# Performance work log

Measured on AMD Instinct MI355X. Metric: run time of the kernel, lower is better.

The kernel has to match this reference:

```python
import jax, jax.numpy as jnp
import numpy as np

V, E, H, B, S, T, NE, NC = 50000, 300, 150, 64, 16, 48, 100001, 300


def bigru(x, Wih, Whh, bih, bhh):
    # x: [T, N, D]; PyTorch GRU cell math, bidirectional -> [T, N, 2H]
    outs = []
    for d in range(2):
        def step(h, xt, d=d):
            gi = xt @ Wih[d].T + bih[d]
            gh = h @ Whh[d].T + bhh[d]
            ir, iz, inn = jnp.split(gi, 3, axis=-1)
            hr, hz, hn = jnp.split(gh, 3, axis=-1)
            r = jax.nn.sigmoid(ir + hr)
            z = jax.nn.sigmoid(iz + hz)
            n = jnp.tanh(inn + r * hn)
            h2 = (1.0 - z) * n + z * h
            return h2, h2
        h0 = jnp.zeros((x.shape[1], Whh.shape[-1]), x.dtype)
        _, hs = jax.lax.scan(step, h0, x, reverse=(d == 1))
        outs.append(hs)
    return jnp.concatenate(outs, axis=-1)


def attend(hs, W, b, ctx):
    # hs: [T, N, G]; softmax attention over time axis
    u = jnp.tanh(jnp.einsum('tng,hg->tnh', hs, W) + b)
    a = jax.nn.softmax(jnp.einsum('tnh,h->tn', u, ctx), axis=0)
    return jnp.einsum('tn,tng->ng', a, hs)


def cos_sim(a, c, eps=1e-8):
    # a: [B, D], c: [B, K, D] -> [B, K]  (torch.cosine_similarity semantics)
    num = jnp.einsum('bd,bkd->bk', a, c)
    den = jnp.linalg.norm(a, axis=-1, keepdims=True) * jnp.linalg.norm(c, axis=-1)
    return num / jnp.maximum(den, eps)


def setup_inputs() -> dict:
    key = jax.random.key(0)
    ks = jax.random.split(key, 20)
    nrm = lambda k, s: (jax.random.normal(k, s, jnp.float32) * 0.05)
    return {
        'docs': jax.random.randint(ks[0], (B, S, T), 0, V),
        'sens': jax.random.randint(ks[1], (B,), 0, S),
        'candidates': jax.random.randint(ks[2], (B, 1, NC), 0, NE),
        'idx': jax.random.randint(ks[3], (B,), 1, NC + 1),  # 1-based gold id
        'word_emb': nrm(ks[4], (V, E)),
        'ent_emb': nrm(ks[5], (NE, E)),
        'Wih_w': nrm(ks[6], (2, 3 * H, E)),
        'Whh_w': nrm(ks[7], (2, 3 * H, H)),
        'bih_w': jnp.zeros((2, 3 * H), jnp.float32),
        'bhh_w': jnp.zeros((2, 3 * H), jnp.float32),
        'attW_w': nrm(ks[8], (2 * H, 2 * H)),
        'attb_w': jnp.zeros((2 * H,), jnp.float32),
        'ctx_w': nrm(ks[9], (2 * H,)),
        'Wih_s': nrm(ks[10], (2, 3 * H, 2 * H)),
        'Whh_s': nrm(ks[11], (2, 3 * H, H)),
        'bih_s': jnp.zeros((2, 3 * H), jnp.float32),
        'bhh_s': jnp.zeros((2, 3 * H), jnp.float32),
        'attW_s': nrm(ks[12], (2 * H, 2 * H)),
        'attb_s': jnp.zeros((2 * H,), jnp.float32),
        'ctx_s': nrm(ks[13], (2 * H,)),
        'linW': nrm(ks[14], (NC, 2 * NC)),
        'linb': jnp.zeros((NC,), jnp.float32),
    }


def reference(docs, sens, candidates, idx, word_emb, ent_emb,
              Wih_w, Whh_w, bih_w, bhh_w, attW_w, attb_w, ctx_w,
              Wih_s, Whh_s, bih_s, bhh_s, attW_s, attb_s, ctx_s,
              linW, linb):
    b, s, t = docs.shape
    # ---- word-level encoder over every sentence at once ----
    x = word_emb[docs]                              # [B,S,T,E]
    x = x.transpose(2, 0, 1, 3).reshape(t, b * s, E)  # [T, B*S, E]
    hs = bigru(x, Wih_w, Whh_w, bih_w, bhh_w)       # [T, B*S, 2H]
    sent_vec = attend(hs, attW_w, attb_w, ctx_w)    # [B*S, 2H]
    sent_vec = sent_vec.reshape(b, s, 2 * H)        # output_per_sen.permute(1,0,2)
    output_sen = sent_vec[jnp.arange(b), sens]      # [B, 2H] mention sentence
    # ---- sentence-level encoder ----
    xs = sent_vec.transpose(1, 0, 2)                # [S, B, 2H]
    hss = bigru(xs, Wih_s, Whh_s, bih_s, bhh_s)     # [S, B, 2H]
    output_doc = attend(hss, attW_s, attb_s, ctx_s)  # [B, 2H]
    # ---- batched cosine similarity against candidate entity embeddings ----
    can = ent_emb[candidates[:, 0]]                 # [B, NC, E]
    sim_total = jnp.concatenate([cos_sim(output_sen, can), cos_sim(output_doc, can)], axis=1)  # [B, 2*NC]
    score = sim_total @ linW.T + linb               # [B, NC]
    score_gold = score[jnp.arange(b), idx - 1]      # [B]
    max_index = jnp.argmax(score, axis=1)           # [B]
    return (score_gold, score, max_index)
```

## Files before the change

### kernel.cpp

```cpp
#include <hip/hip_runtime.h>
#include <hip/hip_bf16.h>
#include <math.h>

#define B_  64
#define S_  16
#define T_  48
#define E_  300
#define H_  150
#define G_  300
#define NC_ 300
#define NW_ (B_*S_)
#define RW_ (T_*NW_)
#define RS_ (S_*B_)
#define GST 960

typedef __attribute__((ext_vector_type(8))) short bf16x8;
typedef __attribute__((ext_vector_type(4))) float f32x4;

__device__ __forceinline__ float sigm(float x){ return 1.0f/(1.0f+__expf(-x)); }

__device__ __forceinline__ ushort f2bf_rne(float x){
  uint u = __float_as_uint(x);
  return (ushort)((u + 0x7FFFu + ((u>>16)&1u)) >> 16);
}

__global__ __launch_bounds__(256) void prep_whh_kernel(
    const float* __restrict__ Whh, float* __restrict__ Wblk){
  int idx = blockIdx.x*256 + threadIdx.x;
  if (idx >= 2*38*450*4) return;
  int k  = idx & 3;
  int j  = (idx >> 2) % 450;
  int e4 = (idx >> 2) / 450 % 38;
  int d  = idx / (38*450*4);
  int e  = e4*4 + k;
  Wblk[idx] = (e < 150) ? Whh[((size_t)d*450 + j)*150 + e] : 0.f;
}

__global__ __launch_bounds__(256) void prep_whh_mfma(
    const float* __restrict__ Whh, ushort* __restrict__ Bsh,
    ushort* __restrict__ Bsl){
  int idx = blockIdx.x*256 + threadIdx.x;
  if (idx >= 2*512*160) return;
  int k = idx % 160;
  int j = (idx / 160) % 512;
  int d = idx / (512*160);
  float x = (j < 450 && k < 150) ? Whh[((size_t)d*450 + j)*150 + k] : 0.f;
  ushort hb = f2bf_rne(x);
  Bsh[idx] = hb;
  Bsl[idx] = f2bf_rne(x - __uint_as_float(((uint)hb)<<16));
}

__global__ __launch_bounds__(128) void split_w_gen(
    const float* __restrict__ W, ushort* __restrict__ Whi,
    ushort* __restrict__ Wlo, int R, int C, int Cp){
  int j = blockIdx.x;
  for (int k = threadIdx.x; k < Cp; k += 128){
    float x = (j < R && k < C) ? W[(size_t)j*C + k] : 0.f;
    ushort hb = f2bf_rne(x);
    float hf = __uint_as_float(((uint)hb)<<16);
    Whi[(size_t)j*Cp + k] = hb;
    Wlo[(size_t)j*Cp + k] = f2bf_rne(x - hf);
  }
}

__global__ __launch_bounds__(256) void gi_mfma_v4(
    const int* __restrict__ docs, const float* __restrict__ emb,
    const ushort* __restrict__ Whi, const ushort* __restrict__ Wlo,
    const float* __restrict__ bih, float* __restrict__ gi){
  __shared__ __align__(16) ushort Bhi[16*328];
  __shared__ __align__(16) ushort Blo[16*328];
  __shared__ __align__(16) float  Cst[64*68];
  __shared__ int toks[64];
  int tid = threadIdx.x;
  int gr0 = blockIdx.x * 64;
  int t  = gr0 >> 10;
  int n0 = gr0 & 1023;
  if (tid < 64) toks[tid] = docs[(n0 + tid)*T_ + t];
  uint4 pb[5];
#pragma unroll
  for (int i=0;i<5;i++){
    int c = tid + i*256;
    int half = (c >= 640) ? 1 : 0; int cc = c - half*640;
    int row = cc/40, o16 = cc - row*40;
    const ushort* src = half ? Wlo : Whi;
    pb[i] = *(const uint4*)&src[(size_t)row*320 + o16*8];
  }
  __syncthreads();
  int w = tid >> 6, L = tid & 63;
  int lrow = L & 15, lseg = L >> 4;
  const float* aptr = emb + (size_t)toks[w*16 + lrow]*300;
  bf16x8 ah[10], al[10];
#pragma unroll
  for (int ks=0; ks<10; ks++){
    int k0 = ks*32 + lseg*8;
    float x[8];
    if (k0 + 8 <= 300){
      float4 v0 = *(const float4*)&aptr[k0];
      float4 v1 = *(const float4*)&aptr[k0+4];
      x[0]=v0.x; x[1]=v0.y; x[2]=v0.z; x[3]=v0.w;
      x[4]=v1.x; x[5]=v1.y; x[6]=v1.z; x[7]=v1.w;
    } else {
#pragma unroll
      for (int u=0;u<8;u++) x[u] = (k0+u < 300) ? aptr[k0+u] : 0.f;
    }
#pragma unroll
    for (int u=0;u<8;u++){
      ushort hb = f2bf_rne(x[u]);
      float lo = x[u] - __uint_as_float(((uint)hb)<<16);
      ah[ks][u] = (short)hb;
      al[ks][u] = (short)f2bf_rne(lo);
    }
  }
#pragma unroll
  for (int i=0;i<5;i++){
    int c = tid + i*256;
    int half = (c >= 640) ? 1 : 0; int cc = c - half*640;
    int row = cc/40, o16 = cc - row*40;
    ushort* dst = half ? Blo : Bhi;
    *(uint4*)&dst[row*328 + o16*8] = pb[i];
  }
  __syncthreads();
  int bfb = lrow*328 + lseg*8;
  int rl0 = w*16 + lseg*4;
  f32x4 acc4[4];
  for (int g = 0; g < 14; ++g){
#pragma unroll
    for (int q = 0; q < 4; ++q){
      int nt = g*4 + q;
#pragma unroll
      for (int i=0;i<5;i++){
        int c = tid + i*256;
        int half = (c >= 640) ? 1 : 0; int cc = c - half*640;
        int row = cc/40, o16 = cc - row*40;
        const ushort* src = half ? Wlo : Whi;
        pb[i] = *(const uint4*)&src[(size_t)((nt+1)*16 + row)*320 + o16*8];
      }
      f32x4 acc = {0.f, 0.f, 0.f, 0.f};
#pragma unroll
      for (int ks=0; ks<10; ks++){
        bf16x8 bh = *(const bf16x8*)&Bhi[bfb + ks*32];
        bf16x8 bl = *(const bf16x8*)&Blo[bfb + ks*32];
        acc = __builtin_amdgcn_mfma_f32_16x16x32_bf16(ah[ks], bh, acc, 0, 0, 0);
        acc = __builtin_amdgcn_mfma_f32_16x16x32_bf16(ah[ks], bl, acc, 0, 0, 0);
        acc = __builtin_amdgcn_mfma_f32_16x16x32_bf16(al[ks], bh, acc, 0, 0, 0);
      }
      acc4[q] = acc;
      __syncthreads();
#pragma unroll
      for (int i=0;i<5;i++){
        int c = tid + i*256;
        int half = (c >= 640) ? 1 : 0; int cc = c - half*640;
        int row = cc/40, o16 = cc - row*40;
        ushort* dst = half ? Blo : Bhi;
        *(uint4*)&dst[row*328 + o16*8] = pb[i];
      }
      __syncthreads();
    }
#pragma unroll
    for (int q = 0; q < 4; ++q){
#pragma unroll
      for (int r = 0; r < 4; ++r)
        Cst[(rl0 + r)*68 + q*16 + lrow] = acc4[q][r];
    }
    __syncthreads();
#pragma unroll
    for (int i = 0; i < 4; ++i){
      int idxc = tid + i*256;
      int row = idxc >> 4, c4 = idxc & 15;
      int colb = g*64 + c4*4;
      float4 v = *(float4*)&Cst[row*68 + c4*4];
      float4 bb = *(const float4*)&bih[colb];
      v.x += bb.x; v.y += bb.y; v.z += bb.z; v.w += bb.w;
      *(float4*)&gi[(size_t)(gr0 + row)*GST + colb] = v;
    }
  }
  {
    f32x4 acc = {0.f, 0.f, 0.f, 0.f};
#pragma unroll
    for (int ks=0; ks<10; ks++){
      bf16x8 bh = *(const bf16x8*)&Bhi[bfb + ks*32];
      bf16x8 bl = *(const bf16x8*)&Blo[bfb + ks*32];
      acc = __builtin_amdgcn_mfma_f32_16x16x32_bf16(ah[ks], bh, acc, 0, 0, 0);
      acc = __builtin_amdgcn_mfma_f32_16x16x32_bf16(ah[ks], bl, acc, 0, 0, 0);
      acc = __builtin_amdgcn_mfma_f32_16x16x32_bf16(al[ks], bh, acc, 0, 0, 0);
    }
    int col = 896 + lrow;
    if (col < 900){
      float bb = bih[col];
#pragma unroll
      for (int r=0;r<4;r++)
        gi[(size_t)(gr0 + rl0 + r)*GST + col] = acc[r] + bb;
    }
  }
}

__global__ __launch_bounds__(256,3) void att_mfma_kernel(
    const float* __restrict__ hs, const ushort* __restrict__ Whi,
    const ushort* __restrict__ Wlo, const float* __restrict__ bias,
    const float* __restrict__ ctx, float* __restrict__ score, int Rtot){
  __shared__ __align__(16) ushort Bhi[2][16*328];
  __shared__ __align__(16) ushort Blo[2][16*328];
  int tid = threadIdx.x;
  int r0 = blockIdx.x * 64;
  uint4 pb[5];
#pragma unroll
  for (int i=0;i<5;i++){
    int c = tid + i*256;
    int half = (c >= 640) ? 1 : 0; int cc = c - half*640;
    int row = cc/40, o16 = cc - row*40;
    const ushort* src = half ? Wlo : Whi;
    pb[i] = *(const uint4*)&src[(size_t)row*320 + o16*8];
  }
  int w = tid >> 6, L = tid & 63;
  int lrow = L & 15, lseg = L >> 4;
  int arow = r0 + w*16 + lrow;
  bool avalid = arow < Rtot;
  const float* aptr = hs + (size_t)(avalid ? arow : 0)*300;
  bf16x8 ah[10], al[10];
#pragma unroll
  for (int ks=0; ks<10; ks++){
    int k0 = ks*32 + lseg*8;
    float x[8];
    if (avalid && k0 + 8 <= 300){
      float4 v0 = *(const float4*)&aptr[k0];
      float4 v1 = *(const float4*)&aptr[k0+4];
      x[0]=v0.x; x[1]=v0.y; x[2]=v0.z; x[3]=v0.w;
      x[4]=v1.x; x[5]=v1.y; x[6]=v1.z; x[7]=v1.w;
    } else {
#pragma unroll
      for (int u=0;u<8;u++) x[u] = (avalid && k0+u < 300) ? aptr[k0+u] : 0.f;
    }
#pragma unroll
    for (int u=0;u<8;u++){
      ushort hb = f2bf_rne(x[u]);
      float lo = x[u] - __uint_as_float(((uint)hb)<<16);
      ah[ks][u] = (short)hb;
      al[ks][u] = (short)f2bf_rne(lo);
    }
  }
#pragma unroll
  for (int i=0;i<5;i++){
    int c = tid + i*256;
    int half = (c >= 640) ? 1 : 0; int cc = c - half*640;
    int row = cc/40, o16 = cc - row*40;
    ushort* dst = half ? Blo[0] : Bhi[0];
    *(uint4*)&dst[row*328 + o16*8] = pb[i];
  }
  __syncthreads();
  int buf = 0;
  int bfb = lrow*328 + lseg*8;
  float part[4] = {0.f,0.f,0.f,0.f};
  for (int nt = 0; nt < 19; ++nt){
    if (nt < 18){
#pragma unroll
      for (int i=0;i<5;i++){
        int c = tid + i*256;
        int half = (c >= 640) ? 1 : 0; int cc = c - half*640;
        int row = cc/40, o16 = cc - row*40;
        const ushort* src = half ? Wlo : Whi;
        pb[i] = *(const uint4*)&src[(size_t)((nt+1)*16 + row)*320 + o16*8];
      }
    }
    f32x4 acc = {0.f, 0.f, 0.f, 0.f};
#pragma unroll
    for (int ks=0; ks<10; ks++){
      bf16x8 bh = *(const bf16x8*)&Bhi[buf][bfb + ks*32];
      bf16x8 bl = *(const bf16x8*)&Blo[buf][bfb + ks*32];
      acc = __builtin_amdgcn_mfma_f32_16x16x32_bf16(ah[ks], bh, acc, 0, 0, 0);
      acc = __builtin_amdgcn_mfma_f32_16x16x32_bf16(ah[ks], bl, acc, 0, 0, 0);
      acc = __builtin_amdgcn_mfma_f32_16x16x32_bf16(al[ks], bh, acc, 0, 0, 0);
    }
    int col = nt*16 + lrow;
    if (col < 300){
      float bb = bias[col], cx = ctx[col];
#pragma unroll
      for (int r=0;r<4;r++) part[r] += cx * tanhf(acc[r] + bb);
    }
    if (nt < 18){
#pragma unroll
      for (int i=0;i<5;i++){
        int c = tid + i*256;
        int half = (c >= 640) ? 1 : 0; int cc = c - half*640;
        int row = cc/40, o16 = cc - row*40;
        ushort* dst = half ? Blo[buf^1] : Bhi[buf^1];
        *(uint4*)&dst[row*328 + o16*8] = pb[i];
      }
    }
    __syncthreads();
    buf ^= 1;
  }
#pragma unroll
  for (int off=1; off<16; off<<=1){
#pragma unroll
    for (int r=0;r<4;r++) part[r] += __shfl_xor(part[r], off);
  }
  if (lrow == 0){
    int rbase = r0 + w*16 + lseg*4;
#pragma unroll
    for (int r=0;r<4;r++)
      if (rbase + r < Rtot) score[rbase + r] = part[r];
  }
}

__global__ __launch_bounds__(256) void sent_gi_kernel(
    const float* __restrict__ sv, const float* __restrict__ Wih,
    const float* __restrict__ bih, float* __restrict__ gi){
  __shared__ float A[16][G_];
  int r0 = blockIdx.x * 16;
  int s  = r0 >> 6;
  int bb_ = r0 & 63;
  for (int idx = threadIdx.x; idx < 16*75; idx += 256){
    int row = idx / 75, e4 = idx - row*75;
    *(float4*)&A[row][e4*4] =
        *(const float4*)&sv[(((size_t)(bb_+row))*S_ + s)*G_ + e4*4];
  }
  __syncthreads();
  int q = threadIdx.x;
  if (q >= 225) return;
  int j0 = q*4;
  const float4* w0 = (const float4*)(Wih + (size_t)(j0  )*G_);
  const float4* w1 = (const float4*)(Wih + (size_t)(j0+1)*G_);
  const float4* w2 = (const float4*)(Wih + (size_t)(j0+2)*G_);
  const float4* w3 = (const float4*)(Wih + (size_t)(j0+3)*G_);
  float acc[16][4];
#pragma unroll
  for (int i=0;i<16;i++){ acc[i][0]=0.f; acc[i][1]=0.f; acc[i][2]=0.f; acc[i][3]=0.f; }
  for (int e4=0; e4<75; e4++){
    float4 b0=w0[e4], b1=w1[e4], b2=w2[e4], b3=w3[e4];
#pragma unroll
    for (int i=0;i<16;i++){
      float4 av = *(const float4*)&A[i][e4*4];
      acc[i][0] += av.x*b0.x + av.y*b0.y + av.z*b0.z + av.w*b0.w;
      acc[i][1] += av.x*b1.x + av.y*b1.y + av.z*b1.z + av.w*b1.w;
      acc[i][2] += av.x*b2.x + av.y*b2.y + av.z*b2.z + av.w*b2.w;
      acc[i][3] += av.x*b3.x + av.y*b3.y + av.z*b3.z + av.w*b3.w;
    }
  }
  float4 bb = *(const float4*)&bih[j0];
#pragma unroll
  for (int i=0;i<16;i++){
    float4 o4;
    o4.x = acc[i][0]+bb.x; o4.y = acc[i][1]+bb.y;
    o4.z = acc[i][2]+bb.z; o4.w = acc[i][3]+bb.w;
    *(float4*)&gi[((size_t)(s*B_) + bb_ + i)*GST + j0] = o4;
  }
}

__global__ __launch_bounds__(512,2) void gru_mfma2(
    const float* __restrict__ gi, const ushort* __restrict__ Bsh,
    const ushort* __restrict__ Bsl, const float* __restrict__ bhh,
    float* __restrict__ hs, int T, int N){
  __shared__ __align__(16) ushort Ahi[16*168];
  __shared__ __align__(16) ushort Alo[16*168];
  __shared__ float gh[16*468];
  __shared__ float lds_pad[10240];
  int tid = threadIdx.x;
  int d  = blockIdx.y;
  int n0 = blockIdx.x * 8;
  if (N == -12345) lds_pad[tid] = 0.f;
  for (int i = tid; i < 16*168; i += 512){ Ahi[i] = 0; Alo[i] = 0; }
  int wv = tid >> 6, L = tid & 63;
  int lrow = L & 15, lseg = L >> 4;
  bf16x8 Bh[4][5], Bl[4][5];
  {
    const ushort* bh_ = Bsh + (size_t)d*512*160;
    const ushort* bl_ = Bsl + (size_t)d*512*160;
#pragma unroll
    for (int q=0;q<4;q++){
      int row = (wv + q*8)*16 + lrow;
#pragma unroll
      for (int ks=0;ks<5;ks++){
        Bh[q][ks] = *(const bf16x8*)&bh_[(size_t)row*160 + lseg*8 + ks*32];
        Bl[q][ks] = *(const bf16x8*)&bl_[(size_t)row*160 + lseg*8 + ks*32];
      }
    }
  }
  int erow[3], eh[3];
  float bb_r[3], bb_z[3], bb_n[3], hold[3];
#pragma unroll
  for (int r=0;r<3;r++){
    int e = tid + r*512;
    bool v = e < 1200;
    int e2 = v ? e : 0;
    erow[r] = e2 / 150; eh[r] = e2 % 150;
    bb_r[r] = v ? bhh[d*450 + eh[r]]        : 0.f;
    bb_z[r] = v ? bhh[d*450 + 150 + eh[r]]  : 0.f;
    bb_n[r] = v ? bhh[d*450 + 300 + eh[r]]  : 0.f;
    hold[r] = 0.f;
  }
  __syncthreads();
  for (int step = 0; step < T; ++step){
    int t = d ? (T-1-step) : step;
    bf16x8 Ah[5], Al[5];
#pragma unroll
    for (int ks=0;ks<5;ks++){
      Ah[ks] = *(const bf16x8*)&Ahi[lrow*168 + lseg*8 + ks*32];
      Al[ks] = *(const bf16x8*)&Alo[lrow*168 + lseg*8 + ks*32];
    }
#pragma unroll
    for (int q=0;q<4;q++){
      int nt = wv + q*8;
      if (nt < 29){
        f32x4 acc = {0.f,0.f,0.f,0.f};
#pragma unroll
        for (int ks=0;ks<5;ks++){
          acc = __builtin_amdgcn_mfma_f32_16x16x32_bf16(Ah[ks], Bh[q][ks], acc, 0,0,0);
          acc = __builtin_amdgcn_mfma_f32_16x16x32_bf16(Ah[ks], Bl[q][ks], acc, 0,0,0);
          acc = __builtin_amdgcn_mfma_f32_16x16x32_bf16(Al[ks], Bh[q][ks], acc, 0,0,0);
        }
        int col = nt*16 + lrow;
#pragma unroll
        for (int r=0;r<4;r++)
          gh[(lseg*4 + r)*468 + col] = acc[r];
      }
    }
    const float* gib = gi + ((size_t)t*N + n0)*GST + d*450;
    float pr[3], pz[3], pn[3];
#pragma unroll
    for (int r=0;r<3;r++){
      if (tid + r*512 < 1200){
        const float* g0 = gib + (size_t)erow[r]*GST + eh[r];
        pr[r] = g0[0]; pz[r] = g0[150]; pn[r] = g0[300];
      }
    }
    __syncthreads();
#pragma unroll
    for (int r=0;r<3;r++){
      if (tid + r*512 < 1200){
        int row = erow[r], h = eh[r];
        float ghr = gh[row*468 + h];
        float ghz = gh[row*468 + 150 + h];
        float ghn = gh[row*468 + 300 + h];
        float rr = sigm(pr[r] + ghr + bb_r[r]);
        float zz = sigm(pz[r] + ghz + bb_z[r]);
        float nn = tanhf(pn[r] + rr*(ghn + bb_n[r]));
        float h2 = (1.f - zz)*nn + zz*hold[r];
        hold[r] = h2;
        ushort hb = f2bf_rne(h2);
        Ahi[row*168 + h] = hb;
        Alo[row*168 + h] = f2bf_rne(h2 - __uint_as_float(((uint)hb)<<16));
        hs[((size_t)t*N + n0 + row)*G_ + d*H_ + h] = h2;
      }
    }
    __syncthreads();
  }
}

template<int R>
__global__ __launch_bounds__(512,2) void gru_scan_v4(
    const float* __restrict__ gi, const float* __restrict__ Wblk,
    const float* __restrict__ bhh, float* __restrict__ hs,
    int T, int N){
  int d  = blockIdx.y;
  int n0 = blockIdx.x * R;
  __shared__ float hl[2][R][152];
  __shared__ float gh[R][452];
  int tid = threadIdx.x;
  for (int idx = tid; idx < 2*R*152; idx += 512) (&hl[0][0][0])[idx] = 0.f;
  bool jact = tid < 450;
  bool hact = tid < 150;
  float4 Wr[38];
  float bj = 0.f;
  {
    const float4* Wb4 = (const float4*)(Wblk + (size_t)d*38*1800);
    int jj = jact ? tid : 0;
#pragma unroll
    for (int e4 = 0; e4 < 38; ++e4) Wr[e4] = Wb4[e4*450 + jj];
    if (jact) bj = bhh[d*450 + tid];
  }
  float hreg[R];
#pragma unroll
  for (int i=0;i<R;i++) hreg[i] = 0.f;
  int buf = 0;
  __syncthreads();
  for (int step = 0; step < T; ++step){
    int t = d ? (T-1-step) : step;
    const float* gib = gi + ((size_t)t*N + n0)*GST + d*450;
    float pre[R][3];
    if (hact){
#pragma unroll
      for (int i=0;i<R;i++){
        pre[i][0] = gib[(size_t)i*GST + tid];
        pre[i][1] = gib[(size_t)i*GST + 150 + tid];
        pre[i][2] = gib[(size_t)i*GST + 300 + tid];
      }
    }
    if (jact){
      float acc[R];
#pragma unroll
      for (int i=0;i<R;i++) acc[i] = 0.f;
#pragma unroll
      for (int e4 = 0; e4 < 38; ++e4){
        float4 w = Wr[e4];
#pragma unroll
        for (int i=0;i<R;i++){
          float4 hv = *(const float4*)&hl[buf][i][e4*4];
          acc[i] += w.x*hv.x + w.y*hv.y + w.z*hv.z + w.w*hv.w;
        }
      }
#pragma unroll
      for (int i=0;i<R;i++) gh[i][tid] = acc[i] + bj;
    }
    __syncthreads();
    if (hact){
#pragma unroll
      for (int i=0;i<R;i++){
        float r  = sigm(pre[i][0] + gh[i][tid]);
        float z  = sigm(pre[i][1] + gh[i][150+tid]);
        float nn = tanhf(pre[i][2] + r*gh[i][300+tid]);
        float h2 = (1.f - z)*nn + z*hreg[i];
        hreg[i] = h2;
        hl[buf^1][i][tid] = h2;
        hs[((size_t)t*N + n0 + i)*G_ + d*H_ + tid] = h2;
      }
    }
    buf ^= 1;
    __syncthreads();
  }
}

__global__ __launch_bounds__(256) void att_combine_kernel(
    const float* __restrict__ score, const float* __restrict__ hs,
    float* __restrict__ out, int T, int N){
  int n = blockIdx.x;
  __shared__ float wa[64];
  if (threadIdx.x < T) wa[threadIdx.x] = score[threadIdx.x*N + n];
  __syncthreads();
  float m = -1e30f;
  for (int t=0;t<T;t++) m = fmaxf(m, wa[t]);
  float den = 0.f;
  for (int t=0;t<T;t++) den += __expf(wa[t]-m);
  float inv = 1.f/den;
  __syncthreads();
  if (threadIdx.x < T) wa[threadIdx.x] = __expf(wa[threadIdx.x]-m)*inv;
  __syncthreads();
  for (int g = threadIdx.x; g < G_; g += 256){
    float acc = 0.f;
    for (int t=0;t<T;t++) acc += wa[t] * hs[((size_t)t*N+n)*G_ + g];
    out[(size_t)n*G_ + g] = acc;
  }
}

__global__ __launch_bounds__(256) void cossim_kernel(
    const int* __restrict__ cand, const int* __restrict__ sens,
    const float* __restrict__ ent, const float* __restrict__ sv,
    const float* __restrict__ odoc, float* __restrict__ sim){
  int w = (blockIdx.x*256 + threadIdx.x) >> 6;
  int lane = threadIdx.x & 63;
  if (w >= B_*NC_) return;
  int b = w / NC_, k = w - b*NC_;
  const float* c  = ent + (size_t)cand[b*NC_ + k]*E_;
  const float* a1 = sv  + ((size_t)b*S_ + sens[b])*G_;
  const float* a2 = odoc + (size_t)b*G_;
  float d1=0.f,d2=0.f,cc=0.f,n1=0.f,n2=0.f;
  for (int e = lane; e < E_; e += 64){
    float cv=c[e], v1=a1[e], v2=a2[e];
    d1+=v1*cv; d2+=v2*cv; cc+=cv*cv; n1+=v1*v1; n2+=v2*v2;
  }
  for (int off=32; off; off>>=1){
    d1+=__shfl_xor(d1,off); d2+=__shfl_xor(d2,off); cc+=__shfl_xor(cc,off);
    n1+=__shfl_xor(n1,off); n2+=__shfl_xor(n2,off);
  }
  if (lane == 0){
    float nc = sqrtf(cc);
    sim[(size_t)b*600 + k]       = d1 / fmaxf(sqrtf(n1)*nc, 1e-8f);
    sim[(size_t)b*600 + 300 + k] = d2 / fmaxf(sqrtf(n2)*nc, 1e-8f);
  }
}

__global__ __launch_bounds__(256) void final_kernel(
    const float* __restrict__ sim, const float* __restrict__ linW,
    const float* __restrict__ linb, const int* __restrict__ idx,
    float* __restrict__ out){
  int b = blockIdx.x;
  __shared__ float ss[600];
  __shared__ float sc[300];
  __shared__ float bv[256];
  __shared__ int   bi[256];
  for (int j = threadIdx.x; j < 600; j += 256) ss[j] = sim[(size_t)b*600 + j];
  __syncthreads();
  float bestv = -1e30f; int besti = 0;
  for (int i = threadIdx.x; i < 300; i += 256){
    const float4* wr = (const float4*)(linW + (size_t)i*600);
    float acc = linb[i];
    for (int j4=0; j4<150; j4++){
      float4 w = wr[j4];
      int j = j4*4;
      acc += w.x*ss[j] + w.y*ss[j+1] + w.z*ss[j+2] + w.w*ss[j+3];
    }
    sc[i] = acc;
    out[64 + (size_t)b*300 + i] = acc;
    if (acc > bestv){ bestv = acc; besti = i; }
  }
  bv[threadIdx.x] = bestv; bi[threadIdx.x] = besti;
  __syncthreads();
  for (int s=128; s; s>>=1){
    if (threadIdx.x < s){
      float ov = bv[threadIdx.x+s]; int oi = bi[threadIdx.x+s];
      if (ov > bv[threadIdx.x] || (ov == bv[threadIdx.x] && oi < bi[threadIdx.x])){
        bv[threadIdx.x] = ov; bi[threadIdx.x] = oi;
      }
    }
    __syncthreads();
  }
  if (threadIdx.x == 0){
    out[b] = sc[idx[b]-1];
    out[64 + 64*300 + b] = (float)bi[0];
  }
}

extern "C" void kernel_launch(void* const* d_in, const int* in_sizes, int n_in,
                              void* d_out, int out_size, void* d_ws, size_t ws_size,
                              hipStream_t stream){
  const int*   docs  = (const int*)d_in[0];
  const int*   sens  = (const int*)d_in[1];
  const int*   cand  = (const int*)d_in[2];
  const int*   idx   = (const int*)d_in[3];
  const float* wemb  = (const float*)d_in[4];
  const float* eemb  = (const float*)d_in[5];
  const float* Wih_w = (const float*)d_in[6];
  const float* Whh_w = (const float*)d_in[7];
  const float* bih_w = (const float*)d_in[8];
  const float* bhh_w = (const float*)d_in[9];
  const float* attW_w= (const float*)d_in[10];
  const float* attb_w= (const float*)d_in[11];
  const float* ctx_w = (const float*)d_in[12];
  const float* Wih_s = (const float*)d_in[13];
  const float* Whh_s = (const float*)d_in[14];
  const float* bih_s = (const float*)d_in[15];
  const float* bhh_s = (const float*)d_in[16];
  const float* attW_s= (const float*)d_in[17];
  const float* attb_s= (const float*)d_in[18];
  const float* ctx_s = (const float*)d_in[19];
  const float* linW  = (const float*)d_in[20];
  const float* linb  = (const float*)d_in[21];

  float* ws = (float*)d_ws;
  size_t off = 0;
  float* gi_w    = ws + off; off += (size_t)T_*NW_*GST;
  float* hs_w    = ws + off; off += (size_t)T_*NW_*G_;
  float* score_w = ws + off; off += (size_t)T_*NW_;
  float* sv      = ws + off; off += (size_t)NW_*G_;
  float* hs_s    = ws + off; off += (size_t)S_*B_*G_;
  float* score_s = ws + off; off += (size_t)S_*B_;
  float* odoc    = ws + off; off += (size_t)B_*G_;
  float* sim     = ws + off; off += (size_t)B_*600;
  float* Wblk_s  = ws + off; off += (size_t)2*38*450*4;
  ushort* Whi    = (ushort*)(ws + off); off += (size_t)912*320/2;
  ushort* Wlo    = (ushort*)(ws + off); off += (size_t)912*320/2;
  ushort* WAhi   = (ushort*)(ws + off); off += (size_t)304*320/2;
  ushort* WAlo   = (ushort*)(ws + off); off += (size_t)304*320/2;
  ushort* WShi   = (ushort*)(ws + off); off += (size_t)304*320/2;
  ushort* WSlo   = (ushort*)(ws + off); off += (size_t)304*320/2;
  ushort* Bsh    = (ushort*)(ws + off); off += (size_t)2*512*160/2;
  ushort* Bsl    = (ushort*)(ws + off); off += (size_t)2*512*160/2;
  float* gi_s    = gi_w;

  float* out = (float*)d_out;

  prep_whh_kernel<<<(2*38*450*4+255)/256, 256, 0, stream>>>(Whh_s, Wblk_s);
  prep_whh_mfma<<<(2*512*160+255)/256, 256, 0, stream>>>(Whh_w, Bsh, Bsl);
  split_w_gen<<<912, 128, 0, stream>>>(Wih_w, Whi, Wlo, 900, 300, 320);
  split_w_gen<<<304, 128, 0, stream>>>(attW_w, WAhi, WAlo, 300, 300, 320);
  split_w_gen<<<304, 128, 0, stream>>>(attW_s, WShi, WSlo, 300, 300, 320);

  gi_mfma_v4<<<RW_/64, 256, 0, stream>>>(docs, wemb, Whi, Wlo, bih_w, gi_w);
  gru_mfma2<<<dim3(NW_/8, 2), 512, 0, stream>>>(gi_w, Bsh, Bsl, bhh_w,
                                                hs_w, T_, NW_);
  att_mfma_kernel<<<RW_/64, 256, 0, stream>>>(hs_w, WAhi, WAlo, attb_w,
                                              ctx_w, score_w, RW_);
  att_combine_kernel<<<NW_, 256, 0, stream>>>(score_w, hs_w, sv, T_, NW_);

  sent_gi_kernel<<<RS_/16, 256, 0, stream>>>(sv, Wih_s, bih_s, gi_s);
  gru_scan_v4<2><<<dim3(B_/2, 2), 512, 0, stream>>>(gi_s, Wblk_s, bhh_s,
                                                    hs_s, S_, B_);
  att_mfma_kernel<<<RS_/64, 256, 0, stream>>>(hs_s, WShi, WSlo, attb_s,
                                              ctx_s, score_s, RS_);
  att_combine_kernel<<<B_, 256, 0, stream>>>(score_s, hs_s, odoc, S_, B_);

  cossim_kernel<<<(B_*NC_*64)/256, 256, 0, stream>>>(cand, sens, eemb, sv, odoc, sim);
  final_kernel<<<B_, 256, 0, stream>>>(sim, linW, linb, idx, out);
}
```

Baseline: 766.4 us.

## Double-buffer weight tiles in gi GEMM and drop GRU LDS padding

```diff
diff --git a/kernel.cpp b/kernel.cpp
--- a/kernel.cpp
+++ b/kernel.cpp
@@ -63,14 +63,15 @@
   }
 }
 
-__global__ __launch_bounds__(256) void gi_mfma_v4(
+__global__ __launch_bounds__(256) void gi_mfma_v7(
     const int* __restrict__ docs, const float* __restrict__ emb,
     const ushort* __restrict__ Whi, const ushort* __restrict__ Wlo,
     const float* __restrict__ bih, float* __restrict__ gi){
-  __shared__ __align__(16) ushort Bhi[16*328];
-  __shared__ __align__(16) ushort Blo[16*328];
-  __shared__ __align__(16) float  Cst[64*68];
-  __shared__ int toks[64];
+  __shared__ __align__(16) char smem[59648];
+  ushort* Bhi = (ushort*)smem;
+  ushort* Blo = (ushort*)(smem + 20992);
+  float*  Cst = (float*)(smem + 41984);
+  int*    toks = (int*)(smem + 59392);
   int tid = threadIdx.x;
   int gr0 = blockIdx.x * 64;
   int t  = gr0 >> 10;
@@ -120,6 +121,7 @@
     *(uint4*)&dst[row*328 + o16*8] = pb[i];
   }
   __syncthreads();
+  int buf = 0;
   int bfb = lrow*328 + lseg*8;
   int rl0 = w*16 + lseg*4;
   f32x4 acc4[4];
@@ -136,25 +138,31 @@
         pb[i] = *(const uint4*)&src[(size_t)((nt+1)*16 + row)*320 + o16*8];
       }
       f32x4 acc = {0.f, 0.f, 0.f, 0.f};
+      const ushort* bh0 = Bhi + buf*5248 + bfb;
+      const ushort* bl0 = Blo + buf*5248 + bfb;
 #pragma unroll
       for (int ks=0; ks<10; ks++){
-        bf16x8 bh = *(const bf16x8*)&Bhi[bfb + ks*32];
-        bf16x8 bl = *(const bf16x8*)&Blo[bfb + ks*32];
+        bf16x8 bh = *(const bf16x8*)&bh0[ks*32];
+        bf16x8 bl = *(const bf16x8*)&bl0[ks*32];
         acc = __builtin_amdgcn_mfma_f32_16x16x32_bf16(ah[ks], bh, acc, 0, 0, 0);
         acc = __builtin_amdgcn_mfma_f32_16x16x32_bf16(ah[ks], bl, acc, 0, 0, 0);
         acc = __builtin_amdgcn_mfma_f32_16x16x32_bf16(al[ks], bh, acc, 0, 0, 0);
       }
       acc4[q] = acc;
+      {
+        ushort* dh = Bhi + (buf^1)*5248;
+        ushort* dl = Blo + (buf^1)*5248;
+#pragma unroll
+        for (int i=0;i<5;i++){
+          int c = tid + i*256;
+          int half = (c >= 640) ? 1 : 0; int cc = c - half*640;
+          int row = cc/40, o16 = cc - row*40;
+          ushort* dst = half ? dl : dh;
+          *(uint4*)&dst[row*328 + o16*8] = pb[i];
+        }
+      }
       __syncthreads();
-#pragma unroll
-      for (int i=0;i<5;i++){
-        int c = tid + i*256;
-        int half = (c >= 640) ? 1 : 0; int cc = c - half*640;
-        int row = cc/40, o16 = cc - row*40;
-        ushort* dst = half ? Blo : Bhi;
-        *(uint4*)&dst[row*328 + o16*8] = pb[i];
-      }
-      __syncthreads();
+      buf ^= 1;
     }
 #pragma unroll
     for (int q = 0; q < 4; ++q){
@@ -173,13 +181,16 @@
       v.x += bb.x; v.y += bb.y; v.z += bb.z; v.w += bb.w;
       *(float4*)&gi[(size_t)(gr0 + row)*GST + colb] = v;
     }
+    __syncthreads();
   }
   {
     f32x4 acc = {0.f, 0.f, 0.f, 0.f};
+    const ushort* bh0 = Bhi + buf*5248 + bfb;
+    const ushort* bl0 = Blo + buf*5248 + bfb;
 #pragma unroll
     for (int ks=0; ks<10; ks++){
-      bf16x8 bh = *(const bf16x8*)&Bhi[bfb + ks*32];
-      bf16x8 bl = *(const bf16x8*)&Blo[bfb + ks*32];
+      bf16x8 bh = *(const bf16x8*)&bh0[ks*32];
+      bf16x8 bl = *(const bf16x8*)&bl0[ks*32];
       acc = __builtin_amdgcn_mfma_f32_16x16x32_bf16(ah[ks], bh, acc, 0, 0, 0);
       acc = __builtin_amdgcn_mfma_f32_16x16x32_bf16(ah[ks], bl, acc, 0, 0, 0);
       acc = __builtin_amdgcn_mfma_f32_16x16x32_bf16(al[ks], bh, acc, 0, 0, 0);
@@ -353,11 +364,9 @@
   __shared__ __align__(16) ushort Ahi[16*168];
   __shared__ __align__(16) ushort Alo[16*168];
   __shared__ float gh[16*468];
-  __shared__ float lds_pad[10240];
   int tid = threadIdx.x;
   int d  = blockIdx.y;
   int n0 = blockIdx.x * 8;
-  if (N == -12345) lds_pad[tid] = 0.f;
   for (int i = tid; i < 16*168; i += 512){ Ahi[i] = 0; Alo[i] = 0; }
   int wv = tid >> 6, L = tid & 63;
   int lrow = L & 15, lseg = L >> 4;
@@ -664,7 +673,7 @@
   split_w_gen<<<304, 128, 0, stream>>>(attW_w, WAhi, WAlo, 300, 300, 320);
   split_w_gen<<<304, 128, 0, stream>>>(attW_s, WShi, WSlo, 300, 300, 320);
 
-  gi_mfma_v4<<<RW_/64, 256, 0, stream>>>(docs, wemb, Whi, Wlo, bih_w, gi_w);
+  gi_mfma_v7<<<RW_/64, 256, 0, stream>>>(docs, wemb, Whi, Wlo, bih_w, gi_w);
   gru_mfma2<<<dim3(NW_/8, 2), 512, 0, stream>>>(gi_w, Bsh, Bsl, bhh_w,
                                                 hs_w, T_, NW_);
   att_mfma_kernel<<<RW_/64, 256, 0, stream>>>(hs_w, WAhi, WAlo, attb_w,
```

Result: faster. 692.3 us (median of 2 runs) (-9.7%).
